# Kernel tuning notes

Measured on AMD Instinct MI355X. Metric: run time of the kernel, lower is better.

## Reference

```python
import jax, jax.numpy as jnp
import numpy as np


def conv1x1(x, w, b):
    # x: [B,Cin,H,W], w: [Cout,Cin], b: [Cout]
    return jnp.einsum('bchw,oc->bohw', x, w) + b[None, :, None, None]


def setup_inputs() -> dict:
    key = jax.random.key(0)
    ks = jax.random.split(key, 10)
    B, Cm, C, H, W = 4, 6, 64, 64, 64
    map1 = jax.random.normal(ks[0], (B, Cm, H, W), jnp.float32)
    map2 = jax.random.normal(ks[1], (B, Cm, H, W), jnp.float32)
    feature_map = jax.random.normal(ks[2], (B, C, H, W), jnp.float32)
    # 1x1 conv params (kaiming-ish scale)
    wb = jax.random.normal(ks[3], (Cm, Cm), jnp.float32) / np.sqrt(Cm)
    bb = jnp.zeros((Cm,), jnp.float32)
    wc = jax.random.normal(ks[4], (Cm, Cm), jnp.float32) / np.sqrt(Cm)
    bc = jnp.zeros((Cm,), jnp.float32)
    wd = jax.random.normal(ks[5], (C, C), jnp.float32) / np.sqrt(C)
    bd = jnp.zeros((C,), jnp.float32)
    alpha = jnp.zeros((1,), jnp.float32)
    return {"map1": map1, "map2": map2, "feature_map": feature_map,
            "wb": wb, "bb": bb, "wc": wc, "bc": bc, "wd": wd, "bd": bd,
            "alpha": alpha}


def reference(map1, map2, feature_map, wb, bb, wc, bc, wd, bd, alpha):
    B, _, H, W = map1.shape
    N = H * W
    # conv1x1 projections, flatten spatial
    feat_b = conv1x1(map1, wb, bb).reshape(B, -1, N).transpose(0, 2, 1)  # [B,N,6]
    feat_c = conv1x1(map2, wc, bc).reshape(B, -1, N)                      # [B,6,N]
    attention_s = jax.nn.softmax(jnp.einsum('bnc,bcm->bnm', feat_b, feat_c), axis=-1)  # [B,N,N]
    feat_d = conv1x1(feature_map, wd, bd).reshape(B, -1, N)               # [B,C,N]
    # bmm with attention_s^T: out[b,c,n] = sum_m feat_d[b,c,m] * attn[b,n,m]
    feat_e = jnp.einsum('bcm,bnm->bcn', feat_d, attention_s).reshape(B, -1, H, W)
    return alpha * feat_e + feature_map
```

## Files before the change

### kernel.cpp

```cpp
#include <hip/hip_runtime.h>
#include <hip/hip_bf16.h>
#include <math.h>


#define BATCH 4
#define CMAP  6
#define CH    64
#define NSP   4096
#define TN    64
#define NT    (NSP/TN)
#define PSTR  72

typedef __attribute__((ext_vector_type(8))) short short8;
typedef __attribute__((ext_vector_type(4))) float f32x4;

#if __has_builtin(__builtin_amdgcn_exp2f)
#define EXP2(x) __builtin_amdgcn_exp2f(x)
#else
#define EXP2(x) exp2f(x)
#endif

__device__ __forceinline__ unsigned f2bf(float f) {
    unsigned u = __float_as_uint(f);
    return (u + 0x7fffu + ((u >> 16) & 1u)) >> 16;
}

#define INVLN2 1.44269504088896f
#define SHIFT_BF16 0xC238u
#define ONE_BF16   0x3F80u


__global__ void proj_kernel(const float* __restrict__ map1, const float* __restrict__ map2,
                            const float* __restrict__ fm,
                            const float* __restrict__ wb, const float* __restrict__ bb,
                            const float* __restrict__ wc, const float* __restrict__ bc,
                            const float* __restrict__ wd, const float* __restrict__ bd,
                            unsigned short* __restrict__ featq8,
                            unsigned short* __restrict__ featk8,
                            unsigned short* __restrict__ featdf)
{
    __shared__ unsigned short vfrag[2048];

    const int b    = blockIdx.z;
    const int half = blockIdx.y;
    const int lane = threadIdx.x & 63;
    const int og   = threadIdx.x >> 6;
    const int n    = blockIdx.x * 64 + lane;

    const int ht = lane >> 5;
    const int mm = lane & 31;
    const int q4 = mm >> 3, jj = mm & 7;
    const int cb_local = og >> 1;
    float vals[CH];
#pragma unroll
    for (int c = 0; c < CH; ++c)
        vals[c] = fm[(size_t)(b*CH + c)*NSP + n];
#pragma unroll
    for (int oi = 0; oi < 8; ++oi) {
        const int o = half*32 + og*8 + oi;
        float a = bd[o];
#pragma unroll
        for (int c = 0; c < CH; ++c)
            a = fmaf(vals[c], wd[o*CH + c], a);
        const int r = (og & 1)*8 + oi;
        vfrag[(ht*2 + cb_local)*512 + (q4*16 + r)*8 + jj] = (unsigned short)f2bf(a);
    }

    if (half == 0 && og == 0) {
        float v1[CMAP], v2[CMAP];
#pragma unroll
        for (int c = 0; c < CMAP; ++c) {
            v1[c] = map1[(size_t)(b*CMAP + c)*NSP + n];
            v2[c] = map2[(size_t)(b*CMAP + c)*NSP + n];
        }
        unsigned qv[CMAP], kv[CMAP];
#pragma unroll
        for (int o = 0; o < CMAP; ++o) {
            float a1 = bb[o], a2 = bc[o];
#pragma unroll
            for (int c = 0; c < CMAP; ++c) {
                a1 = fmaf(v1[c], wb[o*CMAP + c], a1);
                a2 = fmaf(v2[c], wc[o*CMAP + c], a2);
            }
            qv[o] = f2bf(a1 * INVLN2);
            kv[o] = f2bf(a2);
        }
        uint4 qw, kw;
        qw.x = qv[0] | (qv[1] << 16);
        qw.y = qv[2] | (qv[3] << 16);
        qw.z = qv[4] | (qv[5] << 16);
        qw.w = SHIFT_BF16;
        kw.x = kv[0] | (kv[1] << 16);
        kw.y = kv[2] | (kv[3] << 16);
        kw.z = kv[4] | (kv[5] << 16);
        kw.w = ONE_BF16;
        *(uint4*)&featq8[(size_t)(b*NSP + n)*8] = qw;
        *(uint4*)&featk8[(size_t)(b*NSP + n)*8] = kw;
    }

    __syncthreads();

    {
        const int tt = threadIdx.x;
        const uint4 d = *(const uint4*)&vfrag[tt*8];
        const int ht2 = tt >> 7, inner = tt & 127;
        const size_t off = (((size_t)(b*128 + blockIdx.x*2 + ht2)*4) + half*2)*512
                         + (size_t)inner*8;
        *(uint4*)&featdf[off] = d;
    }
}

__global__ __launch_bounds__(256, 2)
void attn_kernel(const unsigned short* __restrict__ featq8,
                 const unsigned short* __restrict__ featk8,
                 const unsigned short* __restrict__ featdf,
                 const float* __restrict__ fm, const float* __restrict__ alpha_p,
                 float* __restrict__ out)
{
    __shared__ unsigned short p_scr[2][4][16*PSTR];

    const int b    = blockIdx.z;
    const int chh  = blockIdx.y;
    const int t    = threadIdx.x;
    const int lane = t & 63, w = t >> 6;
    const int row16 = lane & 15, quad = lane >> 4;
    const int n0w  = blockIdx.x * 64 + w * 16;

    short8 qf = {0,0,0,0,0,0,0,0};
    if (quad == 0)
        qf = *(const short8*)&featq8[(size_t)(b*NSP + n0w + row16)*8];

    const short8 onesb = {(short)ONE_BF16,(short)ONE_BF16,(short)ONE_BF16,(short)ONE_BF16,
                          (short)ONE_BF16,(short)ONE_BF16,(short)ONE_BF16,(short)ONE_BF16};

    const unsigned short* kbase = featk8 + ((size_t)b*NSP + row16)*8 + quad*8;
    const unsigned short* vfb = featdf + ((size_t)b*128*4)*512 + lane*8;
    const int cb0 = chh*2, cb1 = chh*2 + 1;

    const f32x4 zf = {0.f,0.f,0.f,0.f};
    f32x4 acc0 = zf, acc1 = zf, accL = zf;
    const int prow = row16 * PSTR;

#define PAM_DO(pwp, mb, sv)                                                     \
    {                                                                           \
        const float p0 = EXP2(sv[0]), p1 = EXP2(sv[1]);                         \
        const float p2 = EXP2(sv[2]), p3 = EXP2(sv[3]);                         \
        uint2 pp;                                                               \
        pp.x = __builtin_amdgcn_perm(__float_as_uint(p1), __float_as_uint(p0), 0x07060302u); \
        pp.y = __builtin_amdgcn_perm(__float_as_uint(p3), __float_as_uint(p2), 0x07060302u); \
        *(uint2*)((pwp) + (mb)*16) = pp;                                        \
    }

#define LOADK(dst, mt)                                                          \
    dst##0 = *(const short8*)(kbase + ((mt)*TN +  0)*8);                        \
    dst##1 = *(const short8*)(kbase + ((mt)*TN + 16)*8);                        \
    dst##2 = *(const short8*)(kbase + ((mt)*TN + 32)*8);                        \
    dst##3 = *(const short8*)(kbase + ((mt)*TN + 48)*8);

#define LOADV(dst, vt)                                                          \
    dst##0 = *(const short8*)(vfb + (size_t)(((vt)*2 + 0)*4 + cb0)*512);        \
    dst##1 = *(const short8*)(vfb + (size_t)(((vt)*2 + 1)*4 + cb0)*512);        \
    dst##2 = *(const short8*)(vfb + (size_t)(((vt)*2 + 0)*4 + cb1)*512);        \
    dst##3 = *(const short8*)(vfb + (size_t)(((vt)*2 + 1)*4 + cb1)*512);

    short8 kc0, kc1, kc2, kc3, kn0, kn1, kn2, kn3;
    short8 vv0, vv1, vv2, vv3, vn0, vn1, vn2, vn3;
    f32x4 sp0, sp1, sp2, sp3;

    LOADK(kc, 0)
    LOADV(vv, 0)
    LOADV(vn, 1)

    {
        f32x4 a0 = __builtin_amdgcn_mfma_f32_16x16x32_bf16(kc0, qf, zf, 0, 0, 0);
        f32x4 a1 = __builtin_amdgcn_mfma_f32_16x16x32_bf16(kc1, qf, zf, 0, 0, 0);
        f32x4 a2 = __builtin_amdgcn_mfma_f32_16x16x32_bf16(kc2, qf, zf, 0, 0, 0);
        f32x4 a3 = __builtin_amdgcn_mfma_f32_16x16x32_bf16(kc3, qf, zf, 0, 0, 0);
        LOADK(kc, 1)
        unsigned short* pw = &p_scr[0][w][prow + quad*4];
        PAM_DO(pw, 0, a0) PAM_DO(pw, 1, a1) PAM_DO(pw, 2, a2) PAM_DO(pw, 3, a3)
    }
    sp0 = __builtin_amdgcn_mfma_f32_16x16x32_bf16(kc0, qf, zf, 0, 0, 0);
    sp1 = __builtin_amdgcn_mfma_f32_16x16x32_bf16(kc1, qf, zf, 0, 0, 0);
    sp2 = __builtin_amdgcn_mfma_f32_16x16x32_bf16(kc2, qf, zf, 0, 0, 0);
    sp3 = __builtin_amdgcn_mfma_f32_16x16x32_bf16(kc3, qf, zf, 0, 0, 0);
    LOADK(kc, 2)

#pragma unroll 2
    for (int i = 2; i < NT; ++i) {
        const f32x4 t0 = __builtin_amdgcn_mfma_f32_16x16x32_bf16(kc0, qf, zf, 0, 0, 0);
        const f32x4 t1 = __builtin_amdgcn_mfma_f32_16x16x32_bf16(kc1, qf, zf, 0, 0, 0);
        const f32x4 t2 = __builtin_amdgcn_mfma_f32_16x16x32_bf16(kc2, qf, zf, 0, 0, 0);
        const f32x4 t3 = __builtin_amdgcn_mfma_f32_16x16x32_bf16(kc3, qf, zf, 0, 0, 0);

        const unsigned short* pr = &p_scr[i & 1][w][prow + quad*8];
        const short8 a0 = *(const short8*)pr;
        const short8 a1 = *(const short8*)(pr + 32);

        LOADK(kn, i + 1)

        {
            unsigned short* pw = &p_scr[(i + 1) & 1][w][prow + quad*4];
            PAM_DO(pw, 0, sp0) PAM_DO(pw, 1, sp1) PAM_DO(pw, 2, sp2) PAM_DO(pw, 3, sp3)
        }

        acc0 = __builtin_amdgcn_mfma_f32_16x16x32_bf16(a0, vv0, acc0, 0, 0, 0);
        acc0 = __builtin_amdgcn_mfma_f32_16x16x32_bf16(a1, vv1, acc0, 0, 0, 0);
        acc1 = __builtin_amdgcn_mfma_f32_16x16x32_bf16(a0, vv2, acc1, 0, 0, 0);
        acc1 = __builtin_amdgcn_mfma_f32_16x16x32_bf16(a1, vv3, acc1, 0, 0, 0);
        accL = __builtin_amdgcn_mfma_f32_16x16x32_bf16(a0, onesb, accL, 0, 0, 0);
        accL = __builtin_amdgcn_mfma_f32_16x16x32_bf16(a1, onesb, accL, 0, 0, 0);

        vv0 = vn0; vv1 = vn1; vv2 = vn2; vv3 = vn3;
        LOADV(vn, i)
        kc0 = kn0; kc1 = kn1; kc2 = kn2; kc3 = kn3;
        sp0 = t0; sp1 = t1; sp2 = t2; sp3 = t3;
    }

    {
        const unsigned short* pr = &p_scr[0][w][prow + quad*8];
        const short8 a0 = *(const short8*)pr;
        const short8 a1 = *(const short8*)(pr + 32);
        unsigned short* pw = &p_scr[1][w][prow + quad*4];
        PAM_DO(pw, 0, sp0) PAM_DO(pw, 1, sp1) PAM_DO(pw, 2, sp2) PAM_DO(pw, 3, sp3)
        acc0 = __builtin_amdgcn_mfma_f32_16x16x32_bf16(a0, vv0, acc0, 0, 0, 0);
        acc0 = __builtin_amdgcn_mfma_f32_16x16x32_bf16(a1, vv1, acc0, 0, 0, 0);
        acc1 = __builtin_amdgcn_mfma_f32_16x16x32_bf16(a0, vv2, acc1, 0, 0, 0);
        acc1 = __builtin_amdgcn_mfma_f32_16x16x32_bf16(a1, vv3, acc1, 0, 0, 0);
        accL = __builtin_amdgcn_mfma_f32_16x16x32_bf16(a0, onesb, accL, 0, 0, 0);
        accL = __builtin_amdgcn_mfma_f32_16x16x32_bf16(a1, onesb, accL, 0, 0, 0);
        vv0 = vn0; vv1 = vn1; vv2 = vn2; vv3 = vn3;
    }
    {
        const unsigned short* pr = &p_scr[1][w][prow + quad*8];
        const short8 a0 = *(const short8*)pr;
        const short8 a1 = *(const short8*)(pr + 32);
        acc0 = __builtin_amdgcn_mfma_f32_16x16x32_bf16(a0, vv0, acc0, 0, 0, 0);
        acc0 = __builtin_amdgcn_mfma_f32_16x16x32_bf16(a1, vv1, acc0, 0, 0, 0);
        acc1 = __builtin_amdgcn_mfma_f32_16x16x32_bf16(a0, vv2, acc1, 0, 0, 0);
        acc1 = __builtin_amdgcn_mfma_f32_16x16x32_bf16(a1, vv3, acc1, 0, 0, 0);
        accL = __builtin_amdgcn_mfma_f32_16x16x32_bf16(a0, onesb, accL, 0, 0, 0);
        accL = __builtin_amdgcn_mfma_f32_16x16x32_bf16(a1, onesb, accL, 0, 0, 0);
    }
#undef PAM_DO
#undef LOADK
#undef LOADV

    const float alpha = alpha_p[0];
    const float c0 = alpha / (accL[0] + 1e-30f);
    const float c1 = alpha / (accL[1] + 1e-30f);
    const float c2 = alpha / (accL[2] + 1e-30f);
    const float c3 = alpha / (accL[3] + 1e-30f);
#pragma unroll
    for (int cb = 0; cb < 2; ++cb) {
        const int ch = chh*32 + cb*16 + row16;
        const size_t base = (size_t)(b*CH + ch)*NSP + n0w + quad*4;
        const float4 f = *(const float4*)&fm[base];
        const f32x4 a = cb ? acc1 : acc0;
        float4 o;
        o.x = fmaf(c0, a[0], f.x);
        o.y = fmaf(c1, a[1], f.y);
        o.z = fmaf(c2, a[2], f.z);
        o.w = fmaf(c3, a[3], f.w);
        *(float4*)&out[base] = o;
    }
}

extern "C" void kernel_launch(void* const* d_in, const int* in_sizes, int n_in,
                              void* d_out, int out_size, void* d_ws, size_t ws_size,
                              hipStream_t stream)
{
    const float* map1  = (const float*)d_in[0];
    const float* map2  = (const float*)d_in[1];
    const float* fm    = (const float*)d_in[2];
    const float* wb    = (const float*)d_in[3];
    const float* bb    = (const float*)d_in[4];
    const float* wc    = (const float*)d_in[5];
    const float* bc    = (const float*)d_in[6];
    const float* wd    = (const float*)d_in[7];
    const float* bd    = (const float*)d_in[8];
    const float* alpha = (const float*)d_in[9];
    float* out = (float*)d_out;

    unsigned short* featq8 = (unsigned short*)d_ws;
    unsigned short* featk8 = featq8 + (size_t)BATCH*NSP*8;
    unsigned short* featdf = featk8 + (size_t)BATCH*NSP*8;

    proj_kernel<<<dim3(NSP/64, 2, BATCH), 256, 0, stream>>>(
        map1, map2, fm, wb, bb, wc, bc, wd, bd, featq8, featk8, featdf);
    attn_kernel<<<dim3(NSP/64, 2, BATCH), 256, 0, stream>>>(
        featq8, featk8, featdf, fm, alpha, out);
}
```

Before: 123.2 us.

## Split keys across waves and drop per-channel-half duplicated softmax work

```diff
diff --git a/kernel.cpp b/kernel.cpp
--- a/kernel.cpp
+++ b/kernel.cpp
@@ -8,7 +8,7 @@
 #define CH    64
 #define NSP   4096
 #define TN    64
-#define NT    (NSP/TN)
+#define NTH   32
 #define PSTR  72
 
 typedef __attribute__((ext_vector_type(8))) short short8;
@@ -118,13 +118,16 @@
                  float* __restrict__ out)
 {
     __shared__ unsigned short p_scr[2][4][16*PSTR];
-
-    const int b    = blockIdx.z;
-    const int chh  = blockIdx.y;
+    __shared__ float cmb[2][64][21];
+
+    const int b    = blockIdx.y;
     const int t    = threadIdx.x;
     const int lane = t & 63, w = t >> 6;
     const int row16 = lane & 15, quad = lane >> 4;
-    const int n0w  = blockIdx.x * 64 + w * 16;
+    const int qsub  = w >> 1;
+    const int khalf = w & 1;
+    const int n0w  = blockIdx.x * 32 + qsub * 16;
+    const int m0   = khalf * (NSP/2);
 
     short8 qf = {0,0,0,0,0,0,0,0};
     if (quad == 0)
@@ -133,12 +136,13 @@
     const short8 onesb = {(short)ONE_BF16,(short)ONE_BF16,(short)ONE_BF16,(short)ONE_BF16,
                           (short)ONE_BF16,(short)ONE_BF16,(short)ONE_BF16,(short)ONE_BF16};
 
-    const unsigned short* kbase = featk8 + ((size_t)b*NSP + row16)*8 + quad*8;
+    const unsigned short* kbase = featk8 + ((size_t)(b*NSP + m0) + row16)*8 + quad*8;
     const unsigned short* vfb = featdf + ((size_t)b*128*4)*512 + lane*8;
-    const int cb0 = chh*2, cb1 = chh*2 + 1;
+    const int hb = khalf * 64;
 
     const f32x4 zf = {0.f,0.f,0.f,0.f};
-    f32x4 acc0 = zf, acc1 = zf, accL = zf;
+    f32x4 acc[4] = {zf, zf, zf, zf};
+    f32x4 accL = zf;
     const int prow = row16 * PSTR;
 
 #define PAM_DO(pwp, mb, sv)                                                     \
@@ -158,13 +162,30 @@
     dst##3 = *(const short8*)(kbase + ((mt)*TN + 48)*8);
 
 #define LOADV(dst, vt)                                                          \
-    dst##0 = *(const short8*)(vfb + (size_t)(((vt)*2 + 0)*4 + cb0)*512);        \
-    dst##1 = *(const short8*)(vfb + (size_t)(((vt)*2 + 1)*4 + cb0)*512);        \
-    dst##2 = *(const short8*)(vfb + (size_t)(((vt)*2 + 0)*4 + cb1)*512);        \
-    dst##3 = *(const short8*)(vfb + (size_t)(((vt)*2 + 1)*4 + cb1)*512);
+    dst##0 = *(const short8*)(vfb + (size_t)((hb + (vt)*2 + 0)*4 + 0)*512);     \
+    dst##1 = *(const short8*)(vfb + (size_t)((hb + (vt)*2 + 1)*4 + 0)*512);     \
+    dst##2 = *(const short8*)(vfb + (size_t)((hb + (vt)*2 + 0)*4 + 1)*512);     \
+    dst##3 = *(const short8*)(vfb + (size_t)((hb + (vt)*2 + 1)*4 + 1)*512);     \
+    dst##4 = *(const short8*)(vfb + (size_t)((hb + (vt)*2 + 0)*4 + 2)*512);     \
+    dst##5 = *(const short8*)(vfb + (size_t)((hb + (vt)*2 + 1)*4 + 2)*512);     \
+    dst##6 = *(const short8*)(vfb + (size_t)((hb + (vt)*2 + 0)*4 + 3)*512);     \
+    dst##7 = *(const short8*)(vfb + (size_t)((hb + (vt)*2 + 1)*4 + 3)*512);
+
+#define PV(a0_, a1_, vset)                                                      \
+    acc[0] = __builtin_amdgcn_mfma_f32_16x16x32_bf16(a0_, vset##0, acc[0], 0, 0, 0); \
+    acc[0] = __builtin_amdgcn_mfma_f32_16x16x32_bf16(a1_, vset##1, acc[0], 0, 0, 0); \
+    acc[1] = __builtin_amdgcn_mfma_f32_16x16x32_bf16(a0_, vset##2, acc[1], 0, 0, 0); \
+    acc[1] = __builtin_amdgcn_mfma_f32_16x16x32_bf16(a1_, vset##3, acc[1], 0, 0, 0); \
+    acc[2] = __builtin_amdgcn_mfma_f32_16x16x32_bf16(a0_, vset##4, acc[2], 0, 0, 0); \
+    acc[2] = __builtin_amdgcn_mfma_f32_16x16x32_bf16(a1_, vset##5, acc[2], 0, 0, 0); \
+    acc[3] = __builtin_amdgcn_mfma_f32_16x16x32_bf16(a0_, vset##6, acc[3], 0, 0, 0); \
+    acc[3] = __builtin_amdgcn_mfma_f32_16x16x32_bf16(a1_, vset##7, acc[3], 0, 0, 0); \
+    accL   = __builtin_amdgcn_mfma_f32_16x16x32_bf16(a0_, onesb, accL, 0, 0, 0);     \
+    accL   = __builtin_amdgcn_mfma_f32_16x16x32_bf16(a1_, onesb, accL, 0, 0, 0);
 
     short8 kc0, kc1, kc2, kc3, kn0, kn1, kn2, kn3;
-    short8 vv0, vv1, vv2, vv3, vn0, vn1, vn2, vn3;
+    short8 vv0, vv1, vv2, vv3, vv4, vv5, vv6, vv7;
+    short8 vn0, vn1, vn2, vn3, vn4, vn5, vn6, vn7;
     f32x4 sp0, sp1, sp2, sp3;
 
     LOADK(kc, 0)
@@ -187,7 +208,7 @@
     LOADK(kc, 2)
 
 #pragma unroll 2
-    for (int i = 2; i < NT; ++i) {
+    for (int i = 2; i < NTH; ++i) {
         const f32x4 t0 = __builtin_amdgcn_mfma_f32_16x16x32_bf16(kc0, qf, zf, 0, 0, 0);
         const f32x4 t1 = __builtin_amdgcn_mfma_f32_16x16x32_bf16(kc1, qf, zf, 0, 0, 0);
         const f32x4 t2 = __builtin_amdgcn_mfma_f32_16x16x32_bf16(kc2, qf, zf, 0, 0, 0);
@@ -204,14 +225,10 @@
             PAM_DO(pw, 0, sp0) PAM_DO(pw, 1, sp1) PAM_DO(pw, 2, sp2) PAM_DO(pw, 3, sp3)
         }
 
-        acc0 = __builtin_amdgcn_mfma_f32_16x16x32_bf16(a0, vv0, acc0, 0, 0, 0);
-        acc0 = __builtin_amdgcn_mfma_f32_16x16x32_bf16(a1, vv1, acc0, 0, 0, 0);
-        acc1 = __builtin_amdgcn_mfma_f32_16x16x32_bf16(a0, vv2, acc1, 0, 0, 0);
-        acc1 = __builtin_amdgcn_mfma_f32_16x16x32_bf16(a1, vv3, acc1, 0, 0, 0);
-        accL = __builtin_amdgcn_mfma_f32_16x16x32_bf16(a0, onesb, accL, 0, 0, 0);
-        accL = __builtin_amdgcn_mfma_f32_16x16x32_bf16(a1, onesb, accL, 0, 0, 0);
+        PV(a0, a1, vv)
 
         vv0 = vn0; vv1 = vn1; vv2 = vn2; vv3 = vn3;
+        vv4 = vn4; vv5 = vn5; vv6 = vn6; vv7 = vn7;
         LOADV(vn, i)
         kc0 = kn0; kc1 = kn1; kc2 = kn2; kc3 = kn3;
         sp0 = t0; sp1 = t1; sp2 = t2; sp3 = t3;
@@ -223,46 +240,50 @@
         const short8 a1 = *(const short8*)(pr + 32);
         unsigned short* pw = &p_scr[1][w][prow + quad*4];
         PAM_DO(pw, 0, sp0) PAM_DO(pw, 1, sp1) PAM_DO(pw, 2, sp2) PAM_DO(pw, 3, sp3)
-        acc0 = __builtin_amdgcn_mfma_f32_16x16x32_bf16(a0, vv0, acc0, 0, 0, 0);
-        acc0 = __builtin_amdgcn_mfma_f32_16x16x32_bf16(a1, vv1, acc0, 0, 0, 0);
-        acc1 = __builtin_amdgcn_mfma_f32_16x16x32_bf16(a0, vv2, acc1, 0, 0, 0);
-        acc1 = __builtin_amdgcn_mfma_f32_16x16x32_bf16(a1, vv3, acc1, 0, 0, 0);
-        accL = __builtin_amdgcn_mfma_f32_16x16x32_bf16(a0, onesb, accL, 0, 0, 0);
-        accL = __builtin_amdgcn_mfma_f32_16x16x32_bf16(a1, onesb, accL, 0, 0, 0);
+        PV(a0, a1, vv)
         vv0 = vn0; vv1 = vn1; vv2 = vn2; vv3 = vn3;
+        vv4 = vn4; vv5 = vn5; vv6 = vn6; vv7 = vn7;
     }
     {
         const unsigned short* pr = &p_scr[1][w][prow + quad*8];
         const short8 a0 = *(const short8*)pr;
         const short8 a1 = *(const short8*)(pr + 32);
-        acc0 = __builtin_amdgcn_mfma_f32_16x16x32_bf16(a0, vv0, acc0, 0, 0, 0);
-        acc0 = __builtin_amdgcn_mfma_f32_16x16x32_bf16(a1, vv1, acc0, 0, 0, 0);
-        acc1 = __builtin_amdgcn_mfma_f32_16x16x32_bf16(a0, vv2, acc1, 0, 0, 0);
-        acc1 = __builtin_amdgcn_mfma_f32_16x16x32_bf16(a1, vv3, acc1, 0, 0, 0);
-        accL = __builtin_amdgcn_mfma_f32_16x16x32_bf16(a0, onesb, accL, 0, 0, 0);
-        accL = __builtin_amdgcn_mfma_f32_16x16x32_bf16(a1, onesb, accL, 0, 0, 0);
+        PV(a0, a1, vv)
     }
 #undef PAM_DO
 #undef LOADK
 #undef LOADV
-
-    const float alpha = alpha_p[0];
-    const float c0 = alpha / (accL[0] + 1e-30f);
-    const float c1 = alpha / (accL[1] + 1e-30f);
-    const float c2 = alpha / (accL[2] + 1e-30f);
-    const float c3 = alpha / (accL[3] + 1e-30f);
-#pragma unroll
-    for (int cb = 0; cb < 2; ++cb) {
-        const int ch = chh*32 + cb*16 + row16;
-        const size_t base = (size_t)(b*CH + ch)*NSP + n0w + quad*4;
-        const float4 f = *(const float4*)&fm[base];
-        const f32x4 a = cb ? acc1 : acc0;
-        float4 o;
-        o.x = fmaf(c0, a[0], f.x);
-        o.y = fmaf(c1, a[1], f.y);
-        o.z = fmaf(c2, a[2], f.z);
-        o.w = fmaf(c3, a[3], f.w);
-        *(float4*)&out[base] = o;
+#undef PV
+
+    if (khalf == 1) {
+        float* c = cmb[qsub][lane];
+#pragma unroll
+        for (int cb = 0; cb < 4; ++cb)
+            *(float4*)&c[cb*4] = (float4){acc[cb][0], acc[cb][1], acc[cb][2], acc[cb][3]};
+        *(float4*)&c[16] = (float4){accL[0], accL[1], accL[2], accL[3]};
+    }
+    __syncthreads();
+    if (khalf == 0) {
+        const float* c = cmb[qsub][lane];
+        const float4 lo = *(const float4*)&c[16];
+        const float alpha = alpha_p[0];
+        const float c0 = alpha / (accL[0] + lo.x + 1e-30f);
+        const float c1 = alpha / (accL[1] + lo.y + 1e-30f);
+        const float c2 = alpha / (accL[2] + lo.z + 1e-30f);
+        const float c3 = alpha / (accL[3] + 1e-30f + lo.w);
+#pragma unroll
+        for (int cb = 0; cb < 4; ++cb) {
+            const float4 po = *(const float4*)&c[cb*4];
+            const int ch = cb*16 + row16;
+            const size_t base = (size_t)(b*CH + ch)*NSP + n0w + quad*4;
+            const float4 f = *(const float4*)&fm[base];
+            float4 o;
+            o.x = fmaf(c0, acc[cb][0] + po.x, f.x);
+            o.y = fmaf(c1, acc[cb][1] + po.y, f.y);
+            o.z = fmaf(c2, acc[cb][2] + po.z, f.z);
+            o.w = fmaf(c3, acc[cb][3] + po.w, f.w);
+            *(float4*)&out[base] = o;
+        }
     }
 }
 
@@ -288,6 +309,6 @@
 
     proj_kernel<<<dim3(NSP/64, 2, BATCH), 256, 0, stream>>>(
         map1, map2, fm, wb, bb, wc, bc, wd, bd, featq8, featk8, featdf);
-    attn_kernel<<<dim3(NSP/64, 2, BATCH), 256, 0, stream>>>(
+    attn_kernel<<<dim3(NSP/32, BATCH), 256, 0, stream>>>(
         featq8, featk8, featdf, fm, alpha, out);
 }
```

Result: faster. 118.4 us (-3.9%).
